# Kernel tuning notes

Measured on AMD Instinct MI355X. Metric: run time of the kernel, lower is better.

## Reference

```python
import jax, jax.numpy as jnp
import numpy as np

EMBED_DIM = 768
NUM_HEADS = 12
HEAD_DIM = EMBED_DIM // NUM_HEADS
B, N = 4, 2048


def setup_inputs() -> dict:
    key = jax.random.key(0)
    k_x, k_wqkv, k_bqkv, k_wo, k_bo = jax.random.split(key, 5)
    s = 1.0 / np.sqrt(EMBED_DIM)
    return {
        "x": jax.random.normal(k_x, (B, N, EMBED_DIM), dtype=jnp.float32),
        # torch nn.Linear weight layout: [out_features, in_features]
        "w_qkv": jax.random.uniform(k_wqkv, (3 * EMBED_DIM, EMBED_DIM), minval=-s, maxval=s, dtype=jnp.float32),
        "b_qkv": jax.random.uniform(k_bqkv, (3 * EMBED_DIM,), minval=-s, maxval=s, dtype=jnp.float32),
        "w_out": jax.random.uniform(k_wo, (EMBED_DIM, EMBED_DIM), minval=-s, maxval=s, dtype=jnp.float32),
        "b_out": jax.random.uniform(k_bo, (EMBED_DIM,), minval=-s, maxval=s, dtype=jnp.float32),
    }


def reference(x, w_qkv, b_qkv, w_out, b_out):
    Bsz, Nlen, C = x.shape
    # fused QKV projection: [B, N, 3C]
    qkv = jnp.einsum("bnc,oc->bno", x, w_qkv) + b_qkv
    qkv = qkv.reshape(Bsz, Nlen, 3, NUM_HEADS, HEAD_DIM)
    q = qkv[:, :, 0].transpose(0, 2, 1, 3)  # [B, H, N, D]
    k = qkv[:, :, 1].transpose(0, 2, 1, 3)
    v = qkv[:, :, 2].transpose(0, 2, 1, 3)
    scale = 1.0 / np.sqrt(HEAD_DIM).astype(np.float32)
    scores = jnp.einsum("bhqd,bhkd->bhqk", q, k) * scale  # [B, H, N, N]
    attn = jax.nn.softmax(scores, axis=-1)
    ctx = jnp.einsum("bhqk,bhkd->bhqd", attn, v)  # [B, H, N, D]
    ctx = ctx.transpose(0, 2, 1, 3).reshape(Bsz, Nlen, C)
    return jnp.einsum("bnc,oc->bno", ctx, w_out) + b_out
```

## Files before the change

kernel.cpp:

```cpp
#include <hip/hip_runtime.h>
#include <math.h>

typedef __attribute__((ext_vector_type(8))) short bf16x8;
typedef __attribute__((ext_vector_type(4))) float f32x4;
typedef unsigned short u16;

namespace {
constexpr int BATCH = 4, SEQ = 2048, CDIM = 768, NH = 12, HD = 64;
constexpr int MROWS = BATCH * SEQ;
constexpr int KD = CDIM;
constexpr float QSCALE = 0.125f * 1.44269504088896f;
}

__device__ __forceinline__ u16 f2bf(float f) {
  unsigned x = __float_as_uint(f);
  return (u16)((x + 0x7fffu + ((x >> 16) & 1u)) >> 16);
}

__device__ __forceinline__ unsigned pk2bf(float a, float b) {
  unsigned r;
  asm("v_cvt_pk_bf16_f32 %0, %1, %2" : "=v"(r) : "v"(a), "v"(b));
  return r;
}

#if defined(__has_builtin)
#if __has_builtin(__builtin_amdgcn_exp2f)
#define EXP2(x) __builtin_amdgcn_exp2f(x)
#endif
#endif
#ifndef EXP2
#define EXP2(x) exp2f(x)
#endif

#define GLD16(gp, lp)                                                        \
  __builtin_amdgcn_global_load_lds(                                          \
      (const __attribute__((address_space(1))) void*)(gp),                   \
      (__attribute__((address_space(3))) void*)(lp), 16, 0, 0)

__global__ void convert_bf16(const float* __restrict__ x, u16* __restrict__ xb, int nx4,
                             const float* __restrict__ w1, u16* __restrict__ w1b, int n14,
                             const float* __restrict__ w2, u16* __restrict__ w2b, int n24) {
  const int stride = gridDim.x * blockDim.x;
  const int t0 = blockIdx.x * blockDim.x + threadIdx.x;
  for (int i = t0; i < nx4; i += stride) {
    float4 v = ((const float4*)x)[i];
    ushort4 o; o.x = f2bf(v.x); o.y = f2bf(v.y); o.z = f2bf(v.z); o.w = f2bf(v.w);
    ((ushort4*)xb)[i] = o;
  }
  for (int i = t0; i < n14; i += stride) {
    float4 v = ((const float4*)w1)[i];
    ushort4 o; o.x = f2bf(v.x); o.y = f2bf(v.y); o.z = f2bf(v.z); o.w = f2bf(v.w);
    ((ushort4*)w1b)[i] = o;
  }
  for (int i = t0; i < n24; i += stride) {
    float4 v = ((const float4*)w2)[i];
    ushort4 o; o.x = f2bf(v.x); o.y = f2bf(v.y); o.z = f2bf(v.z); o.w = f2bf(v.w);
    ((ushort4*)w2b)[i] = o;
  }
}

template <int MODE>
__global__ __launch_bounds__(256, 3) void gemm_bf16(
    const u16* __restrict__ A, const u16* __restrict__ Bw,
    const float* __restrict__ bias, float* __restrict__ outf,
    u16* __restrict__ qws, u16* __restrict__ kws, u16* __restrict__ vws) {
  __shared__ u16 smem[2 * 128 * 64];
  u16* As = smem;
  u16* Bs = smem + 128 * 64;
  const int t = threadIdx.x;
  const int w = t >> 6, l = t & 63, g = l >> 4, li = l & 15;
  const int wm = w >> 1, wn = w & 1;
  const int lin = blockIdx.x;
  const int rowb = ((lin & 7) << 3) | ((lin >> 3) & 7);
  const int colb = lin >> 6;
  const int row0 = rowb * 128, col0 = colb * 128;

  const int srow = w * 32 + (l >> 3);
  const int skc = (l & 7) ^ (l >> 3);
  const u16* gA = A + (size_t)(row0 + srow) * KD + skc * 8;
  const u16* gB = Bw + (size_t)(col0 + srow) * KD + skc * 8;

  f32x4 acc[4][4];
#pragma unroll
  for (int a = 0; a < 4; ++a)
#pragma unroll
    for (int c = 0; c < 4; ++c) acc[a][c] = {0.f, 0.f, 0.f, 0.f};

#define GSTAGE(k0_)                                                           \
  do {                                                                        \
    _Pragma("unroll")                                                         \
    for (int j = 0; j < 4; ++j) {                                             \
      GLD16(gA + (size_t)8 * j * KD + (k0_), &As[(w * 32 + 8 * j) * 64]);     \
      GLD16(gB + (size_t)8 * j * KD + (k0_), &Bs[(w * 32 + 8 * j) * 64]);     \
    }                                                                         \
  } while (0)

  constexpr int NK = KD / 64;
  GSTAGE(0);
  asm volatile("s_waitcnt vmcnt(0)" ::: "memory");
  __builtin_amdgcn_sched_barrier(0);
  __builtin_amdgcn_s_barrier();
  __builtin_amdgcn_sched_barrier(0);

  for (int kk = 0; kk < NK; ++kk) {
    bf16x8 af[4][2], bfr[4][2];
#pragma unroll
    for (int mi = 0; mi < 4; ++mi) {
      const int r = wm * 64 + mi * 16 + li;
#pragma unroll
      for (int ks = 0; ks < 2; ++ks)
        af[mi][ks] = *(const bf16x8*)&As[r * 64 + (((ks * 4 + g) ^ (li & 7)) * 8)];
    }
#pragma unroll
    for (int ni = 0; ni < 4; ++ni) {
      const int r = wn * 64 + ni * 16 + li;
#pragma unroll
      for (int ks = 0; ks < 2; ++ks)
        bfr[ni][ks] = *(const bf16x8*)&Bs[r * 64 + (((ks * 4 + g) ^ (li & 7)) * 8)];
    }
    asm volatile("s_waitcnt lgkmcnt(0)" ::: "memory");
    __builtin_amdgcn_sched_barrier(0);
    __builtin_amdgcn_s_barrier();
    __builtin_amdgcn_sched_barrier(0);

    if (kk + 1 < NK) GSTAGE((kk + 1) * 64);

    __builtin_amdgcn_s_setprio(1);
#pragma unroll
    for (int ni = 0; ni < 4; ++ni)
#pragma unroll
      for (int mi = 0; mi < 4; ++mi) {
        acc[mi][ni] = __builtin_amdgcn_mfma_f32_16x16x32_bf16(af[mi][0], bfr[ni][0], acc[mi][ni], 0, 0, 0);
        acc[mi][ni] = __builtin_amdgcn_mfma_f32_16x16x32_bf16(af[mi][1], bfr[ni][1], acc[mi][ni], 0, 0, 0);
      }
    __builtin_amdgcn_s_setprio(0);

    if (kk + 1 < NK) {
      asm volatile("s_waitcnt vmcnt(0)" ::: "memory");
      __builtin_amdgcn_sched_barrier(0);
      __builtin_amdgcn_s_barrier();
      __builtin_amdgcn_sched_barrier(0);
    }
  }
#undef GSTAGE

  float bsr[4];
#pragma unroll
  for (int ni = 0; ni < 4; ++ni) bsr[ni] = bias[col0 + wn * 64 + ni * 16 + li];
  const int bidx = row0 >> 11;
  const int nseq0 = row0 & (SEQ - 1);

  __syncthreads();

  if (MODE == 1) {
    float* Cf = (float*)smem;
#pragma unroll
    for (int p = 0; p < 4; ++p) {
      if (wm == (p >> 1)) {
#pragma unroll
        for (int m2 = 0; m2 < 2; ++m2) {
          const int mi = (p & 1) * 2 + m2;
#pragma unroll
          for (int ni = 0; ni < 4; ++ni)
#pragma unroll
            for (int i = 0; i < 4; ++i)
              Cf[(m2 * 16 + 4 * g + i) * 132 + wn * 64 + ni * 16 + li] =
                  acc[mi][ni][i] + bsr[ni];
        }
      }
      __syncthreads();
#pragma unroll
      for (int j = 0; j < 4; ++j) {
        const int fid = t + 256 * j;
        const int r = fid >> 5, c4 = (fid & 31) * 4;
        *(float4*)(outf + (size_t)(row0 + p * 32 + r) * CDIM + col0 + c4) =
            *(const float4*)&Cf[r * 132 + c4];
      }
      __syncthreads();
    }
  } else {
#pragma unroll
    for (int hc = 0; hc < 2; ++hc) {
      const int nb = col0 + hc * 64;
      const int s = nb / CDIM;
      const int h = (nb % CDIM) / HD;
      if (wn == hc) {
        if (s < 2) {
          const float qs = (s == 0) ? QSCALE : 1.f;
#pragma unroll
          for (int mi = 0; mi < 4; ++mi)
#pragma unroll
            for (int ni = 0; ni < 4; ++ni)
#pragma unroll
              for (int i = 0; i < 4; ++i)
                smem[(wm * 64 + mi * 16 + 4 * g + i) * 72 + ni * 16 + li] =
                    f2bf((acc[mi][ni][i] + bsr[ni]) * qs);
        } else {
#pragma unroll
          for (int mi = 0; mi < 4; ++mi)
#pragma unroll
            for (int ni = 0; ni < 4; ++ni)
#pragma unroll
              for (int i = 0; i < 4; ++i)
                smem[(ni * 16 + li) * 136 + wm * 64 + mi * 16 + 4 * g + i] =
                    f2bf(acc[mi][ni][i] + bsr[ni]);
        }
      }
      __syncthreads();
      if (s < 2) {
        u16* dst = (s == 0 ? qws : kws) + ((size_t)(bidx * NH + h) * SEQ + nseq0) * HD;
        const int r = t >> 3, c = (t & 7) * 8;
#pragma unroll
        for (int rd = 0; rd < 4; ++rd)
          *(uint4*)(dst + (size_t)(r + 32 * rd) * HD + c) =
              *(const uint4*)&smem[(r + 32 * rd) * 72 + c];
      } else {
        u16* dst = vws + (size_t)(bidx * NH + h) * HD * SEQ + nseq0;
        const int d = t >> 4, c = (t & 15) * 8;
#pragma unroll
        for (int rd = 0; rd < 4; ++rd)
          *(uint4*)(dst + (size_t)(d + 16 * rd) * SEQ + c) =
              *(const uint4*)&smem[(d + 16 * rd) * 136 + c];
      }
      __syncthreads();
    }
  }
}

__global__ __launch_bounds__(256, 3) void attn_mfma(
    const u16* __restrict__ qws, const u16* __restrict__ kws,
    const u16* __restrict__ vws, u16* __restrict__ ctx) {
  __shared__ u16 Ks[2][64 * 64];
  __shared__ u16 Vs[2][64 * 64];
  __shared__ u16 Ps[4 * 32 * 72];
  const int t = threadIdx.x;
  const int w = t >> 6, l = t & 63, g = l >> 4, li = l & 15;
  const int q0 = blockIdx.x * 128;
  const int h = blockIdx.y, b = blockIdx.z;
  const size_t bh = (size_t)b * NH + h;
  const u16* qb = qws + bh * SEQ * HD;
  const u16* kb = kws + bh * SEQ * HD;
  const u16* vb = vws + bh * HD * SEQ;

  bf16x8 qf[2][2];
#pragma unroll
  for (int qt = 0; qt < 2; ++qt)
#pragma unroll
    for (int ks = 0; ks < 2; ++ks)
      qf[qt][ks] = *(const bf16x8*)(qb + (size_t)(q0 + w * 32 + qt * 16 + li) * HD + ks * 32 + g * 8);
  asm volatile("s_waitcnt vmcnt(0)" ::: "memory");
  __builtin_amdgcn_sched_barrier(0);

  f32x4 acc[4][2];
#pragma unroll
  for (int dt = 0; dt < 4; ++dt)
#pragma unroll
    for (int qt = 0; qt < 2; ++qt) acc[dt][qt] = {0.f, 0.f, 0.f, 0.f};
  float lrun[2] = {0.f, 0.f};

  const int srow8 = l >> 3;
  const int skc = (l & 7) ^ srow8;
  const u16* gK = kb + (size_t)(w * 16 + srow8) * HD + skc * 8;
  const u16* gV = vb + (size_t)(w * 16 + srow8) * SEQ + skc * 8;
  u16* Pw = Ps + w * 32 * 72;

  constexpr int NT = SEQ / 64;

#define STAGE(kt_, buf_)                                                          \
  do {                                                                            \
    const int key0_ = (kt_) * 64;                                                 \
    GLD16(gK + (size_t)(key0_ + 0) * HD, &Ks[buf_][(w * 16 + 0) * 64]);           \
    GLD16(gV + (size_t)0 * SEQ + key0_, &Vs[buf_][(w * 16 + 0) * 64]);            \
    GLD16(gK + (size_t)(key0_ + 8) * HD, &Ks[buf_][(w * 16 + 8) * 64]);           \
    GLD16(gV + (size_t)8 * SEQ + key0_, &Vs[buf_][(w * 16 + 8) * 64]);            \
  } while (0)

  STAGE(0, 0);
  STAGE(1, 1);
  asm volatile("s_waitcnt vmcnt(4)" ::: "memory");
  __builtin_amdgcn_sched_barrier(0);
  __builtin_amdgcn_s_barrier();
  __builtin_amdgcn_sched_barrier(0);

  const f32x4 Z = {0.f, 0.f, 0.f, 0.f};

  for (int kt = 0; kt < NT; ++kt) {
    const int cur = kt & 1;
    const u16* KsC = Ks[cur];
    const u16* VsC = Vs[cur];

    f32x4 S[4][2];
    __builtin_amdgcn_s_setprio(1);
#pragma unroll
    for (int kb4 = 0; kb4 < 4; ++kb4) {
      bf16x8 kf0 = *(const bf16x8*)&KsC[(kb4 * 16 + li) * 64 + ((g ^ (li & 7)) * 8)];
      bf16x8 kf1 = *(const bf16x8*)&KsC[(kb4 * 16 + li) * 64 + (((4 + g) ^ (li & 7)) * 8)];
#pragma unroll
      for (int qt = 0; qt < 2; ++qt) {
        S[kb4][qt] = __builtin_amdgcn_mfma_f32_16x16x32_bf16(kf0, qf[qt][0], Z, 0, 0, 0);
        S[kb4][qt] = __builtin_amdgcn_mfma_f32_16x16x32_bf16(kf1, qf[qt][1], S[kb4][qt], 0, 0, 0);
      }
    }
    __builtin_amdgcn_s_setprio(0);

#pragma unroll
    for (int qt = 0; qt < 2; ++qt) {
      float rs = 0.f;
#pragma unroll
      for (int kb4 = 0; kb4 < 4; ++kb4) {
        const float p0 = EXP2(S[kb4][qt][0]);
        const float p1 = EXP2(S[kb4][qt][1]);
        const float p2 = EXP2(S[kb4][qt][2]);
        const float p3 = EXP2(S[kb4][qt][3]);
        rs += (p0 + p1) + (p2 + p3);
        uint2 pk;
        pk.x = pk2bf(p0, p1);
        pk.y = pk2bf(p2, p3);
        *(uint2*)&Pw[(qt * 16 + li) * 72 + ((kb4 ^ (li & 3)) * 16) + 4 * g] = pk;
      }
      lrun[qt] += rs;
    }

    bf16x8 vf[4][2];
#pragma unroll
    for (int dt = 0; dt < 4; ++dt) {
      vf[dt][0] = *(const bf16x8*)&VsC[(dt * 16 + li) * 64 + ((g ^ (li & 7)) * 8)];
      vf[dt][1] = *(const bf16x8*)&VsC[(dt * 16 + li) * 64 + (((4 + g) ^ (li & 7)) * 8)];
    }
    bf16x8 pf[2][2];
#pragma unroll
    for (int qt = 0; qt < 2; ++qt)
#pragma unroll
      for (int ks = 0; ks < 2; ++ks) {
        const int slot = (ks * 2 + (g >> 1)) ^ (li & 3);
        pf[qt][ks] = *(const bf16x8*)&Pw[(qt * 16 + li) * 72 + slot * 16 + (g & 1) * 8];
      }

    __builtin_amdgcn_s_setprio(1);
#pragma unroll
    for (int dt = 0; dt < 4; ++dt)
#pragma unroll
      for (int qt = 0; qt < 2; ++qt) {
        acc[dt][qt] = __builtin_amdgcn_mfma_f32_16x16x32_bf16(vf[dt][0], pf[qt][0], acc[dt][qt], 0, 0, 0);
        acc[dt][qt] = __builtin_amdgcn_mfma_f32_16x16x32_bf16(vf[dt][1], pf[qt][1], acc[dt][qt], 0, 0, 0);
      }
    __builtin_amdgcn_s_setprio(0);

    if (kt + 1 < NT) {
      asm volatile("s_waitcnt vmcnt(0)" ::: "memory");
      __builtin_amdgcn_sched_barrier(0);
      __builtin_amdgcn_s_barrier();
      __builtin_amdgcn_sched_barrier(0);
      if (kt + 2 < NT) STAGE(kt + 2, cur);
    }
  }
#undef STAGE

#pragma unroll
  for (int qt = 0; qt < 2; ++qt) {
    lrun[qt] += __shfl_xor(lrun[qt], 16);
    lrun[qt] += __shfl_xor(lrun[qt], 32);
  }
  float inv[2] = {1.f / lrun[0], 1.f / lrun[1]};
#pragma unroll
  for (int qt = 0; qt < 2; ++qt)
#pragma unroll
    for (int dt = 0; dt < 4; ++dt) {
      uint2 pk;
      pk.x = pk2bf(acc[dt][qt][0] * inv[qt], acc[dt][qt][1] * inv[qt]);
      pk.y = pk2bf(acc[dt][qt][2] * inv[qt], acc[dt][qt][3] * inv[qt]);
      *(uint2*)&Ps[(w * 32 + qt * 16 + li) * 72 + dt * 16 + 4 * g] = pk;
    }
  __syncthreads();
  {
    const int r = t >> 3, c = (t & 7) * 8;
#pragma unroll
    for (int rd = 0; rd < 4; ++rd)
      *(uint4*)(ctx + ((size_t)b * SEQ + q0 + r + 32 * rd) * CDIM + h * HD + c) =
          *(const uint4*)&Ps[(r + 32 * rd) * 72 + c];
  }
}

extern "C" void kernel_launch(void* const* d_in, const int* in_sizes, int n_in,
                              void* d_out, int out_size, void* d_ws, size_t ws_size,
                              hipStream_t stream) {
  (void)in_sizes; (void)n_in; (void)out_size; (void)ws_size;
  const float* x     = (const float*)d_in[0];
  const float* w_qkv = (const float*)d_in[1];
  const float* b_qkv = (const float*)d_in[2];
  const float* w_out = (const float*)d_in[3];
  const float* b_out = (const float*)d_in[4];
  float* out = (float*)d_out;

  u16* xb    = (u16*)d_ws;
  u16* wqkvb = xb + (size_t)MROWS * KD;
  u16* wob   = wqkvb + (size_t)3 * CDIM * KD;
  u16* qb    = wob + (size_t)CDIM * KD;
  const size_t QS = (size_t)BATCH * NH * SEQ * HD;
  u16* kb   = qb + QS;
  u16* vb   = kb + QS;
  u16* ctxb = vb + QS;

  hipLaunchKernelGGL(convert_bf16, dim3(2048), dim3(256), 0, stream,
                     x, xb, MROWS * KD / 4,
                     w_qkv, wqkvb, 3 * CDIM * KD / 4,
                     w_out, wob, CDIM * KD / 4);
  hipLaunchKernelGGL((gemm_bf16<0>), dim3((MROWS / 128) * (3 * CDIM / 128)), dim3(256), 0,
                     stream, xb, wqkvb, b_qkv, nullptr, qb, kb, vb);
  hipLaunchKernelGGL(attn_mfma, dim3(SEQ / 128, NH, BATCH), dim3(256), 0, stream,
                     qb, kb, vb, ctxb);
  hipLaunchKernelGGL((gemm_bf16<1>), dim3((MROWS / 128) * (CDIM / 128)), dim3(256), 0,
                     stream, ctxb, wob, b_out, out, nullptr, nullptr, nullptr);
}
```

Before: 201.8 us.

## Use 8-wave GEMM blocks with simple load-sync-compute loop and inline v_exp_f32

The projection GEMM now runs 512 threads (8 waves) per 128x128 tile, so each wave owns a 32x64 sub-tile with half the accumulators. The hand-scheduled prefetch of the next K slice, with its setprio hints, is replaced by a plain sync-load-sync-compute loop. The idea is to hide memory latency through more resident waves rather than explicit overlap, at the risk of exposing load latency inside each block. The attention softmax also swaps the exp2 builtin for inline v_exp_f32 assembly.

After: 203.7 us. About the same (+0.9%).

```diff
diff --git a/kernel.cpp b/kernel.cpp
--- a/kernel.cpp
+++ b/kernel.cpp
@@ -23,14 +23,11 @@
   return r;
 }
 
-#if defined(__has_builtin)
-#if __has_builtin(__builtin_amdgcn_exp2f)
-#define EXP2(x) __builtin_amdgcn_exp2f(x)
-#endif
-#endif
-#ifndef EXP2
-#define EXP2(x) exp2f(x)
-#endif
+__device__ __forceinline__ float exp2asm(float x) {
+  float r;
+  asm("v_exp_f32 %0, %1" : "=v"(r) : "v"(x));
+  return r;
+}
 
 #define GLD16(gp, lp)                                                        \
   __builtin_amdgcn_global_load_lds(                                          \
@@ -60,7 +57,7 @@
 }
 
 template <int MODE>
-__global__ __launch_bounds__(256, 3) void gemm_bf16(
+__global__ __launch_bounds__(512, 4) void gemm_bf16(
     const u16* __restrict__ A, const u16* __restrict__ Bw,
     const float* __restrict__ bias, float* __restrict__ outf,
     u16* __restrict__ qws, u16* __restrict__ kws, u16* __restrict__ vws) {
@@ -75,38 +72,36 @@
   const int colb = lin >> 6;
   const int row0 = rowb * 128, col0 = colb * 128;
 
-  const int srow = w * 32 + (l >> 3);
+  const int srow = w * 16 + (l >> 3);
   const int skc = (l & 7) ^ (l >> 3);
   const u16* gA = A + (size_t)(row0 + srow) * KD + skc * 8;
   const u16* gB = Bw + (size_t)(col0 + srow) * KD + skc * 8;
 
-  f32x4 acc[4][4];
-#pragma unroll
-  for (int a = 0; a < 4; ++a)
+  f32x4 acc[2][4];
+#pragma unroll
+  for (int a = 0; a < 2; ++a)
 #pragma unroll
     for (int c = 0; c < 4; ++c) acc[a][c] = {0.f, 0.f, 0.f, 0.f};
 
 #define GSTAGE(k0_)                                                           \
   do {                                                                        \
     _Pragma("unroll")                                                         \
-    for (int j = 0; j < 4; ++j) {                                             \
-      GLD16(gA + (size_t)8 * j * KD + (k0_), &As[(w * 32 + 8 * j) * 64]);     \
-      GLD16(gB + (size_t)8 * j * KD + (k0_), &Bs[(w * 32 + 8 * j) * 64]);     \
+    for (int j = 0; j < 2; ++j) {                                             \
+      GLD16(gA + (size_t)8 * j * KD + (k0_), &As[(w * 16 + 8 * j) * 64]);     \
+      GLD16(gB + (size_t)8 * j * KD + (k0_), &Bs[(w * 16 + 8 * j) * 64]);     \
     }                                                                         \
   } while (0)
 
   constexpr int NK = KD / 64;
-  GSTAGE(0);
-  asm volatile("s_waitcnt vmcnt(0)" ::: "memory");
-  __builtin_amdgcn_sched_barrier(0);
-  __builtin_amdgcn_s_barrier();
-  __builtin_amdgcn_sched_barrier(0);
-
   for (int kk = 0; kk < NK; ++kk) {
-    bf16x8 af[4][2], bfr[4][2];
-#pragma unroll
-    for (int mi = 0; mi < 4; ++mi) {
-      const int r = wm * 64 + mi * 16 + li;
+    __syncthreads();
+    GSTAGE(kk * 64);
+    __syncthreads();
+
+    bf16x8 af[2][2], bfr[4][2];
+#pragma unroll
+    for (int mi = 0; mi < 2; ++mi) {
+      const int r = wm * 32 + mi * 16 + li;
 #pragma unroll
       for (int ks = 0; ks < 2; ++ks)
         af[mi][ks] = *(const bf16x8*)&As[r * 64 + (((ks * 4 + g) ^ (li & 7)) * 8)];
@@ -118,29 +113,13 @@
       for (int ks = 0; ks < 2; ++ks)
         bfr[ni][ks] = *(const bf16x8*)&Bs[r * 64 + (((ks * 4 + g) ^ (li & 7)) * 8)];
     }
-    asm volatile("s_waitcnt lgkmcnt(0)" ::: "memory");
-    __builtin_amdgcn_sched_barrier(0);
-    __builtin_amdgcn_s_barrier();
-    __builtin_amdgcn_sched_barrier(0);
-
-    if (kk + 1 < NK) GSTAGE((kk + 1) * 64);
-
-    __builtin_amdgcn_s_setprio(1);
 #pragma unroll
     for (int ni = 0; ni < 4; ++ni)
 #pragma unroll
-      for (int mi = 0; mi < 4; ++mi) {
+      for (int mi = 0; mi < 2; ++mi) {
         acc[mi][ni] = __builtin_amdgcn_mfma_f32_16x16x32_bf16(af[mi][0], bfr[ni][0], acc[mi][ni], 0, 0, 0);
         acc[mi][ni] = __builtin_amdgcn_mfma_f32_16x16x32_bf16(af[mi][1], bfr[ni][1], acc[mi][ni], 0, 0, 0);
       }
-    __builtin_amdgcn_s_setprio(0);
-
-    if (kk + 1 < NK) {
-      asm volatile("s_waitcnt vmcnt(0)" ::: "memory");
-      __builtin_amdgcn_sched_barrier(0);
-      __builtin_amdgcn_s_barrier();
-      __builtin_amdgcn_sched_barrier(0);
-    }
   }
 #undef GSTAGE
 
@@ -156,22 +135,20 @@
     float* Cf = (float*)smem;
 #pragma unroll
     for (int p = 0; p < 4; ++p) {
-      if (wm == (p >> 1)) {
-#pragma unroll
-        for (int m2 = 0; m2 < 2; ++m2) {
-          const int mi = (p & 1) * 2 + m2;
+      if (wm == p) {
+#pragma unroll
+        for (int mi = 0; mi < 2; ++mi)
 #pragma unroll
           for (int ni = 0; ni < 4; ++ni)
 #pragma unroll
             for (int i = 0; i < 4; ++i)
-              Cf[(m2 * 16 + 4 * g + i) * 132 + wn * 64 + ni * 16 + li] =
+              Cf[(mi * 16 + 4 * g + i) * 132 + wn * 64 + ni * 16 + li] =
                   acc[mi][ni][i] + bsr[ni];
-        }
       }
       __syncthreads();
 #pragma unroll
-      for (int j = 0; j < 4; ++j) {
-        const int fid = t + 256 * j;
+      for (int j = 0; j < 2; ++j) {
+        const int fid = t + 512 * j;
         const int r = fid >> 5, c4 = (fid & 31) * 4;
         *(float4*)(outf + (size_t)(row0 + p * 32 + r) * CDIM + col0 + c4) =
             *(const float4*)&Cf[r * 132 + c4];
@@ -188,21 +165,21 @@
         if (s < 2) {
           const float qs = (s == 0) ? QSCALE : 1.f;
 #pragma unroll
-          for (int mi = 0; mi < 4; ++mi)
+          for (int mi = 0; mi < 2; ++mi)
 #pragma unroll
             for (int ni = 0; ni < 4; ++ni)
 #pragma unroll
               for (int i = 0; i < 4; ++i)
-                smem[(wm * 64 + mi * 16 + 4 * g + i) * 72 + ni * 16 + li] =
+                smem[(wm * 32 + mi * 16 + 4 * g + i) * 72 + ni * 16 + li] =
                     f2bf((acc[mi][ni][i] + bsr[ni]) * qs);
         } else {
 #pragma unroll
-          for (int mi = 0; mi < 4; ++mi)
+          for (int mi = 0; mi < 2; ++mi)
 #pragma unroll
             for (int ni = 0; ni < 4; ++ni)
 #pragma unroll
               for (int i = 0; i < 4; ++i)
-                smem[(ni * 16 + li) * 136 + wm * 64 + mi * 16 + 4 * g + i] =
+                smem[(ni * 16 + li) * 136 + wm * 32 + mi * 16 + 4 * g + i] =
                     f2bf(acc[mi][ni][i] + bsr[ni]);
         }
       }
@@ -211,16 +188,16 @@
         u16* dst = (s == 0 ? qws : kws) + ((size_t)(bidx * NH + h) * SEQ + nseq0) * HD;
         const int r = t >> 3, c = (t & 7) * 8;
 #pragma unroll
-        for (int rd = 0; rd < 4; ++rd)
-          *(uint4*)(dst + (size_t)(r + 32 * rd) * HD + c) =
-              *(const uint4*)&smem[(r + 32 * rd) * 72 + c];
+        for (int rd = 0; rd < 2; ++rd)
+          *(uint4*)(dst + (size_t)(r + 64 * rd) * HD + c) =
+              *(const uint4*)&smem[(r + 64 * rd) * 72 + c];
       } else {
         u16* dst = vws + (size_t)(bidx * NH + h) * HD * SEQ + nseq0;
         const int d = t >> 4, c = (t & 15) * 8;
 #pragma unroll
-        for (int rd = 0; rd < 4; ++rd)
-          *(uint4*)(dst + (size_t)(d + 16 * rd) * SEQ + c) =
-              *(const uint4*)&smem[(d + 16 * rd) * 136 + c];
+        for (int rd = 0; rd < 2; ++rd)
+          *(uint4*)(dst + (size_t)(d + 32 * rd) * SEQ + c) =
+              *(const uint4*)&smem[(d + 32 * rd) * 136 + c];
       }
       __syncthreads();
     }
@@ -308,10 +285,10 @@
       float rs = 0.f;
 #pragma unroll
       for (int kb4 = 0; kb4 < 4; ++kb4) {
-        const float p0 = EXP2(S[kb4][qt][0]);
-        const float p1 = EXP2(S[kb4][qt][1]);
-        const float p2 = EXP2(S[kb4][qt][2]);
-        const float p3 = EXP2(S[kb4][qt][3]);
+        const float p0 = exp2asm(S[kb4][qt][0]);
+        const float p1 = exp2asm(S[kb4][qt][1]);
+        const float p2 = exp2asm(S[kb4][qt][2]);
+        const float p3 = exp2asm(S[kb4][qt][3]);
         rs += (p0 + p1) + (p2 + p3);
         uint2 pk;
         pk.x = pk2bf(p0, p1);
@@ -405,10 +382,10 @@
                      x, xb, MROWS * KD / 4,
                      w_qkv, wqkvb, 3 * CDIM * KD / 4,
                      w_out, wob, CDIM * KD / 4);
-  hipLaunchKernelGGL((gemm_bf16<0>), dim3((MROWS / 128) * (3 * CDIM / 128)), dim3(256), 0,
+  hipLaunchKernelGGL((gemm_bf16<0>), dim3((MROWS / 128) * (3 * CDIM / 128)), dim3(512), 0,
                      stream, xb, wqkvb, b_qkv, nullptr, qb, kb, vb);
   hipLaunchKernelGGL(attn_mfma, dim3(SEQ / 128, NH, BATCH), dim3(256), 0, stream,
                      qb, kb, vb, ctxb);
-  hipLaunchKernelGGL((gemm_bf16<1>), dim3((MROWS / 128) * (CDIM / 128)), dim3(256), 0,
+  hipLaunchKernelGGL((gemm_bf16<1>), dim3((MROWS / 128) * (CDIM / 128)), dim3(512), 0,
                      stream, ctxb, wob, b_out, out, nullptr, nullptr, nullptr);
 }
```
